# Kernel optimization log

Measured on AMD Instinct MI355X. Metric: run time of the kernel, lower is better.

Reference implementation:

```python
import jax, jax.numpy as jnp
import numpy as np

N, E = 20000, 320000
IN_DIM, CODE_DIM, HIDDEN, HEADS, NREL = 896, 768, 256, 4, 5
CH = HIDDEN // HEADS
CODE_WEIGHT = 3.0
NEG_SLOPE = 0.2


def _gat_layer(h, src, dst, W, att_src, att_dst, bias):
    # h: [N, HIDDEN]; src/dst already include self-loops. Eval mode -> no dropout.
    n = h.shape[0]
    x = (h @ W).reshape(n, HEADS, CH)                      # [N,H,C]
    a_src = (x * att_src).sum(-1)                          # [N,H]
    a_dst = (x * att_dst).sum(-1)                          # [N,H]
    alpha = jax.nn.leaky_relu(a_src[src] + a_dst[dst], NEG_SLOPE)  # [E',H]
    amax = jax.ops.segment_max(alpha, dst, num_segments=n)
    amax = jnp.where(jnp.isfinite(amax), amax, 0.0)
    ex = jnp.exp(alpha - amax[dst])
    denom = jax.ops.segment_sum(ex, dst, num_segments=n)
    coef = ex / denom[dst]                                 # segment softmax over in-neighbors
    msg = x[src] * coef[:, :, None]                        # [E',H,C]
    out = jax.ops.segment_sum(msg, dst, num_segments=n)    # [N,H,C]
    return out.reshape(n, HEADS * CH) + bias


def setup_inputs() -> dict:
    key = jax.random.key(0)
    ks = jax.random.split(key, 20)
    def glorot(k, shape):
        fan_in = shape[0]
        return jax.random.normal(k, shape, jnp.float32) / jnp.sqrt(jnp.asarray(fan_in, jnp.float32))
    inp = {
        "x": jax.random.normal(ks[0], (N, IN_DIM), jnp.float32),
        "edge_index": jax.random.randint(ks[1], (2, E), 0, N, jnp.int32),
        "edge_type": jax.random.randint(ks[2], (E,), 0, NREL, jnp.int32),
        "edge_weight": jax.random.uniform(ks[3], (E,), jnp.float32),
        "rel_emb": jax.random.normal(ks[4], (NREL, HIDDEN), jnp.float32),
        "Wp": glorot(ks[5], (IN_DIM, HIDDEN)),
        "bp": jnp.zeros((HIDDEN,), jnp.float32),
        "W1": glorot(ks[6], (HIDDEN, HIDDEN)),
        "att_src1": glorot(ks[7], (HEADS, CH)) * 0.1,
        "att_dst1": glorot(ks[8], (HEADS, CH)) * 0.1,
        "b1": jnp.zeros((HIDDEN,), jnp.float32),
        "W2": glorot(ks[9], (HIDDEN, HIDDEN)),
        "att_src2": glorot(ks[10], (HEADS, CH)) * 0.1,
        "att_dst2": glorot(ks[11], (HEADS, CH)) * 0.1,
        "b2": jnp.zeros((HIDDEN,), jnp.float32),
        "Wo": glorot(ks[12], (HIDDEN, 1)),
        "bo": jnp.zeros((1,), jnp.float32),
    }
    return inp


def reference(x, edge_index, edge_type, edge_weight, rel_emb, Wp, bp,
              W1, att_src1, att_dst1, b1, W2, att_src2, att_dst2, b2, Wo, bo):
    # feature reorder + code reweighting
    x_code = x[:, :CODE_DIM]
    x_num = x[:, CODE_DIM:]
    xc = jnp.concatenate([x_num, CODE_WEIGHT * x_code], axis=-1)
    h = jax.nn.relu(xc @ Wp + bp)                          # [N,HIDDEN]

    src, dst = edge_index[0], edge_index[1]
    # relational message + index_add scatter
    rel = rel_emb[edge_type] * edge_weight[:, None]        # [E,HIDDEN]
    msg = h[src] + rel
    h = h + jax.ops.segment_sum(msg, dst, num_segments=N)

    # GATConv adds self-loops by default
    loop = jnp.arange(N, dtype=src.dtype)
    src_sl = jnp.concatenate([src, loop])
    dst_sl = jnp.concatenate([dst, loop])

    h = _gat_layer(h, src_sl, dst_sl, W1, att_src1, att_dst1, b1)
    h = _gat_layer(h, src_sl, dst_sl, W2, att_src2, att_dst2, b2)
    score = (h @ Wo + bo)[:, 0]                            # [N]
    return score
```

## Files before the change

kernel.cpp:

```cpp
#include <hip/hip_runtime.h>
#include <hip/hip_bf16.h>

#define N_NODES 20000
#define E_EDGES 320000

typedef __attribute__((ext_vector_type(8))) short s8v;
typedef __attribute__((ext_vector_type(4))) float f4v;

__device__ __forceinline__ float lrelu(float v){ return v > 0.f ? v : 0.2f * v; }

__device__ __forceinline__ float bitf(unsigned short u){
  union { unsigned int i; float f; } v; v.i = ((unsigned int)u) << 16; return v.f;
}
__device__ __forceinline__ float4 bf4(const unsigned short* p){
  ushort4 u = *(const ushort4*)p;
  return make_float4(bitf(u.x), bitf(u.y), bitf(u.z), bitf(u.w));
}
__device__ __forceinline__ unsigned short bfhi(float v){
  union{float f; unsigned u;} a; a.f = v;
  unsigned r = a.u + 0x7FFFu + ((a.u >> 16) & 1u);
  return (unsigned short)(r >> 16);
}
__device__ __forceinline__ float bf2f(unsigned short h){
  union{unsigned u; float f;} a; a.u = ((unsigned)h) << 16; return a.f;
}
__device__ __forceinline__ void split2(float v0, float v1, unsigned& hu, unsigned& lu){
  __hip_bfloat162 h2 = __float22bfloat162_rn(make_float2(v0, v1));
  unsigned h; __builtin_memcpy(&h, &h2, 4);
  union{unsigned u; float f;} c0, c1;
  c0.u = h << 16;
  c1.u = h & 0xFFFF0000u;
  __hip_bfloat162 l2 = __float22bfloat162_rn(make_float2(v0 - c0.f, v1 - c1.f));
  unsigned l; __builtin_memcpy(&l, &l2, 4);
  hu = h; lu = l;
}
__device__ __forceinline__ void gl_lds16(const void* g, void* l){
  __builtin_amdgcn_global_load_lds(
      (const __attribute__((address_space(1))) unsigned int*)g,
      (__attribute__((address_space(3))) unsigned int*)l, 16, 0, 0);
}

__global__ __launch_bounds__(256) void k_count(const int* __restrict__ dst, int* __restrict__ deg, int E){
  int e = blockIdx.x * 256 + threadIdx.x;
  if (e < E) atomicAdd(&deg[dst[e]], 1);
}

__global__ __launch_bounds__(256) void k_scan(const int* __restrict__ deg, int* __restrict__ off,
                                              int* __restrict__ cur, int n){
  __shared__ int part[256];
  __shared__ int base[257];
  int tid = threadIdx.x;
  int chunk = (n + 255) / 256;
  int st = tid * chunk;
  int en = st + chunk; if (en > n) en = n;
  int s = 0;
  for (int i = st; i < en; ++i) s += deg[i];
  part[tid] = s;
  __syncthreads();
  if (tid == 0){
    int a = 0;
    for (int i = 0; i < 256; ++i){ base[i] = a; a += part[i]; }
    base[256] = a;
  }
  __syncthreads();
  int a = base[tid];
  for (int i = st; i < en; ++i){ off[i] = a; cur[i] = 0; a += deg[i]; }
  if (tid == 0) off[n] = base[256];
}

__global__ __launch_bounds__(256) void k_fill(const int* __restrict__ src, const int* __restrict__ dst,
                       const int* __restrict__ ety, const float* __restrict__ ew,
                       const int* __restrict__ off, int* __restrict__ cur,
                       int* __restrict__ csrc, int* __restrict__ cet, float* __restrict__ cw, int E){
  int e = blockIdx.x * 256 + threadIdx.x;
  if (e < E){
    int d = dst[e];
    int p = atomicAdd(&cur[d], 1);
    int i = off[d] + p;
    csrc[i] = src[e];
    cet[i]  = ety[e];
    cw[i]   = ew[e];
  }
}

__global__ __launch_bounds__(64) void k_prep(const float* __restrict__ W, unsigned short* __restrict__ Bp, int K){
  int kt = blockIdx.x;
  int n  = blockIdx.y * 64 + threadIdx.x;
  unsigned short hi[32], lo[32];
#pragma unroll
  for (int kk = 0; kk < 32; ++kk){
    float v = W[(size_t)(kt * 32 + kk) * 256 + n];
    unsigned short h = bfhi(v);
    hi[kk] = h;
    lo[kk] = bfhi(v - bf2f(h));
  }
  size_t plane = (size_t)(K >> 5) * 256 * 32;
  size_t b = ((size_t)kt * 256 + n) * 32;
#pragma unroll
  for (int kk = 0; kk < 32; ++kk){
    Bp[b + kk]         = hi[kk];
    Bp[plane + b + kk] = lo[kk];
  }
}

__global__ __launch_bounds__(128, 4) void k_mmp(
    const float* __restrict__ A, const unsigned short* __restrict__ Bp,
    const float* __restrict__ bias, unsigned short* __restrict__ Cout)
{
  constexpr int KT = 28;
  __shared__ unsigned short AhB[2][32 * 40];
  __shared__ unsigned short AlB[2][32 * 40];

  const int tid  = threadIdx.x;
  const int lane = tid & 63;
  const int wn   = tid >> 6;
  const int l15  = lane & 15;
  const int kg   = lane >> 4;
  const int m0   = blockIdx.x * 32;
  const int n0   = blockIdx.y * 128;
  const size_t planeB = (size_t)KT * 256 * 32;

  f4v acc[2][4];
#pragma unroll
  for (int f = 0; f < 2; ++f)
#pragma unroll
    for (int g = 0; g < 4; ++g)
#pragma unroll
      for (int r = 0; r < 4; ++r) acc[f][g][r] = 0.f;

  const int arow = tid >> 2;
  const int aj   = tid & 3;
  const int gr   = m0 + arow;

  auto loadA = [&](float* v, int kt){
    int c = kt * 32 + aj * 8;
    const float* sp; float sc;
    if (c < 128){ sp = A + (size_t)gr * 896 + (768 + c); sc = 1.f; }
    else        { sp = A + (size_t)gr * 896 + (c - 128); sc = 3.f; }
    float4 f0 = *(const float4*)sp;
    float4 f1 = *(const float4*)(sp + 4);
    v[0]=f0.x*sc; v[1]=f0.y*sc; v[2]=f0.z*sc; v[3]=f0.w*sc;
    v[4]=f1.x*sc; v[5]=f1.y*sc; v[6]=f1.z*sc; v[7]=f1.w*sc;
  };
  auto writeLDS = [&](const float* v, int buf){
    union { unsigned u[4]; s8v s; } hv, lv;
#pragma unroll
    for (int p = 0; p < 4; ++p)
      split2(v[2*p], v[2*p+1], hv.u[p], lv.u[p]);
    *(s8v*)&AhB[buf][arow * 40 + aj * 8] = hv.s;
    *(s8v*)&AlB[buf][arow * 40 + aj * 8] = lv.s;
  };

  float av[8];
  loadA(av, 0);
  writeLDS(av, 0);
  loadA(av, 1);

  int cur = 0;
#pragma unroll 1
  for (int kt = 0; kt < KT; ++kt){
    __syncthreads();
    if (kt + 1 < KT) writeLDS(av, cur ^ 1);
    if (kt + 2 < KT) loadA(av, kt + 2);
    s8v bh[4], bl[4];
#pragma unroll
    for (int g = 0; g < 4; ++g){
      const unsigned short* bp2 = Bp + ((size_t)kt * 256 + n0 + wn * 64 + g * 16 + l15) * 32 + kg * 8;
      bh[g] = *(const s8v*)bp2;
      bl[g] = *(const s8v*)(bp2 + planeB);
    }
    s8v ah[2], al[2];
#pragma unroll
    for (int f = 0; f < 2; ++f){
      int row = f * 16 + l15;
      ah[f] = *(const s8v*)&AhB[cur][row * 40 + kg * 8];
      al[f] = *(const s8v*)&AlB[cur][row * 40 + kg * 8];
    }
#pragma unroll
    for (int f = 0; f < 2; ++f)
#pragma unroll
      for (int g = 0; g < 4; ++g){
        acc[f][g] = __builtin_amdgcn_mfma_f32_16x16x32_bf16(ah[f], bh[g], acc[f][g], 0, 0, 0);
        acc[f][g] = __builtin_amdgcn_mfma_f32_16x16x32_bf16(ah[f], bl[g], acc[f][g], 0, 0, 0);
        acc[f][g] = __builtin_amdgcn_mfma_f32_16x16x32_bf16(al[f], bh[g], acc[f][g], 0, 0, 0);
      }
    cur ^= 1;
  }

#pragma unroll
  for (int f = 0; f < 2; ++f){
#pragma unroll
    for (int g = 0; g < 4; ++g){
      int col = n0 + wn * 64 + g * 16 + l15;
      float bb = bias[col];
#pragma unroll
      for (int r = 0; r < 4; ++r){
        int row = m0 + f * 16 + kg * 4 + r;
        float v = fmaxf(acc[f][g][r] + bb, 0.f);
        Cout[(size_t)row * 256 + col] = bfhi(v);
      }
    }
  }
}

__global__ __launch_bounds__(256, 2) void k_mmh(
    const unsigned short* __restrict__ Ahi, const unsigned short* __restrict__ Alo,
    const unsigned short* __restrict__ Bp, unsigned short* __restrict__ Cout,
    const float* __restrict__ attS, const float* __restrict__ attD,
    float* __restrict__ aS, float* __restrict__ aD)
{
  constexpr int KT = 8;
  __shared__ alignas(16) unsigned char Abuf[2][4096];

  const int tid  = threadIdx.x;
  const int lane = tid & 63;
  const int w    = tid >> 6;
  const int l15  = lane & 15;
  const int kg   = lane >> 4;
  const int m0   = blockIdx.x * 32;
  const size_t planeB = (size_t)KT * 256 * 32;

  f4v acc[2][4];
#pragma unroll
  for (int f = 0; f < 2; ++f)
#pragma unroll
    for (int g = 0; g < 4; ++g)
#pragma unroll
      for (int r = 0; r < 4; ++r) acc[f][g][r] = 0.f;

  auto stage = [&](int buf, int kt){
    int s   = tid;
    int p   = s >> 7;
    int sp  = s & 127;
    int row = sp >> 2;
    int kcp = sp & 3;
    int kc  = kcp ^ (row & 3);
    const unsigned short* basep = p ? Alo : Ahi;
    const unsigned short* gp = basep + (size_t)(m0 + row) * 256 + kt * 32 + kc * 8;
    gl_lds16(gp, &Abuf[buf][w * 1024]);
  };
  auto readFrags = [&](s8v* ah, s8v* al, int buf){
#pragma unroll
    for (int f = 0; f < 2; ++f){
      int row = f * 16 + l15;
      int kc  = kg ^ (row & 3);
      ah[f] = *(const s8v*)&Abuf[buf][row * 64 + kc * 16];
      al[f] = *(const s8v*)&Abuf[buf][2048 + row * 64 + kc * 16];
    }
  };
  auto loadB = [&](s8v* bh, s8v* bl, int kt){
#pragma unroll
    for (int g = 0; g < 4; ++g){
      const unsigned short* bp2 = Bp + ((size_t)kt * 256 + w * 64 + g * 16 + l15) * 32 + kg * 8;
      bh[g] = *(const s8v*)bp2;
      bl[g] = *(const s8v*)(bp2 + planeB);
    }
  };
  auto doMFMA = [&](const s8v* ah, const s8v* al, const s8v* bh, const s8v* bl){
#pragma unroll
    for (int f = 0; f < 2; ++f)
#pragma unroll
      for (int g = 0; g < 4; ++g){
        acc[f][g] = __builtin_amdgcn_mfma_f32_16x16x32_bf16(ah[f], bh[g], acc[f][g], 0, 0, 0);
        acc[f][g] = __builtin_amdgcn_mfma_f32_16x16x32_bf16(ah[f], bl[g], acc[f][g], 0, 0, 0);
        acc[f][g] = __builtin_amdgcn_mfma_f32_16x16x32_bf16(al[f], bh[g], acc[f][g], 0, 0, 0);
      }
  };

  s8v bh[4], bl[4];
  stage(0, 0);
  loadB(bh, bl, 0);
  __syncthreads();

  int cur = 0;
#pragma unroll 1
  for (int kt = 0; kt < KT; ++kt){
    if (kt + 1 < KT) stage(cur ^ 1, kt + 1);
    s8v ah[2], al[2];
    readFrags(ah, al, cur);
    s8v nbh[4], nbl[4];
    if (kt + 1 < KT) loadB(nbh, nbl, kt + 1);
    doMFMA(ah, al, bh, bl);
    if (kt + 1 < KT){
#pragma unroll
      for (int g = 0; g < 4; ++g){ bh[g] = nbh[g]; bl[g] = nbl[g]; }
    }
    __syncthreads();
    cur ^= 1;
  }

#pragma unroll
  for (int f = 0; f < 2; ++f){
#pragma unroll
    for (int g = 0; g < 4; ++g){
      int col = w * 64 + g * 16 + l15;
#pragma unroll
      for (int r = 0; r < 4; ++r){
        int row = m0 + f * 16 + kg * 4 + r;
        Cout[(size_t)row * 256 + col] = bfhi(acc[f][g][r]);
      }
    }
  }

  {
    const int head = w;
    float sv[4], dv[4];
#pragma unroll
    for (int g = 0; g < 4; ++g){
      int col = w * 64 + g * 16 + l15;
      sv[g] = attS[col];
      dv[g] = attD[col];
    }
#pragma unroll
    for (int f = 0; f < 2; ++f){
#pragma unroll
      for (int r = 0; r < 4; ++r){
        float ps = acc[f][0][r]*sv[0] + acc[f][1][r]*sv[1] + acc[f][2][r]*sv[2] + acc[f][3][r]*sv[3];
        float pd = acc[f][0][r]*dv[0] + acc[f][1][r]*dv[1] + acc[f][2][r]*dv[2] + acc[f][3][r]*dv[3];
#pragma unroll
        for (int mm = 1; mm < 16; mm <<= 1){
          ps += __shfl_xor(ps, mm, 64);
          pd += __shfl_xor(pd, mm, 64);
        }
        int row = m0 + f * 16 + kg * 4 + r;
        if (l15 == 0){
          aS[(size_t)row * 4 + head] = ps;
          aD[(size_t)row * 4 + head] = pd;
        }
      }
    }
  }
}

__global__ __launch_bounds__(256) void k_agg(
    const unsigned short* __restrict__ h0, const int* __restrict__ off,
    const int* __restrict__ csrc, const int* __restrict__ cet, const float* __restrict__ cw,
    const float* __restrict__ rel,
    unsigned short* __restrict__ h1hi, unsigned short* __restrict__ h1lo, int N)
{
  __shared__ int srcs[4][128];
  const int wv = threadIdx.x >> 6;
  const int n  = blockIdx.x * 4 + wv;
  if (n >= N) return;
  const int lane = threadIdx.x & 63;
  const int c0 = lane * 4;
  const int s0 = off[n], s1 = off[n + 1];
  const int deg = s1 - s0;
  const int nc = deg < 128 ? deg : 128;

  float w0=0.f, w1=0.f, w2=0.f, w3=0.f, w4=0.f;
  for (int base = 0; base < deg; base += 64){
    int ci = base + lane;
    if (ci < deg){
      int e = s0 + ci;
      int s = csrc[e];
      int t = cet[e];
      float wg = cw[e];
      if (ci < 128) srcs[wv][ci] = s;
      w0 += (t == 0) ? wg : 0.f;
      w1 += (t == 1) ? wg : 0.f;
      w2 += (t == 2) ? wg : 0.f;
      w3 += (t == 3) ? wg : 0.f;
      w4 += (t == 4) ? wg : 0.f;
    }
  }
#pragma unroll
  for (int mm = 1; mm < 64; mm <<= 1){
    w0 += __shfl_xor(w0, mm, 64);
    w1 += __shfl_xor(w1, mm, 64);
    w2 += __shfl_xor(w2, mm, 64);
    w3 += __shfl_xor(w3, mm, 64);
    w4 += __shfl_xor(w4, mm, 64);
  }
  asm volatile("s_waitcnt lgkmcnt(0)" ::: "memory");

  float4 acc = bf4(&h0[(size_t)n * 256 + c0]);
  { float4 R = *(const float4*)&rel[0 * 256 + c0];
    acc.x = fmaf(w0, R.x, acc.x); acc.y = fmaf(w0, R.y, acc.y);
    acc.z = fmaf(w0, R.z, acc.z); acc.w = fmaf(w0, R.w, acc.w); }
  { float4 R = *(const float4*)&rel[1 * 256 + c0];
    acc.x = fmaf(w1, R.x, acc.x); acc.y = fmaf(w1, R.y, acc.y);
    acc.z = fmaf(w1, R.z, acc.z); acc.w = fmaf(w1, R.w, acc.w); }
  { float4 R = *(const float4*)&rel[2 * 256 + c0];
    acc.x = fmaf(w2, R.x, acc.x); acc.y = fmaf(w2, R.y, acc.y);
    acc.z = fmaf(w2, R.z, acc.z); acc.w = fmaf(w2, R.w, acc.w); }
  { float4 R = *(const float4*)&rel[3 * 256 + c0];
    acc.x = fmaf(w3, R.x, acc.x); acc.y = fmaf(w3, R.y, acc.y);
    acc.z = fmaf(w3, R.z, acc.z); acc.w = fmaf(w3, R.w, acc.w); }
  { float4 R = *(const float4*)&rel[4 * 256 + c0];
    acc.x = fmaf(w4, R.x, acc.x); acc.y = fmaf(w4, R.y, acc.y);
    acc.z = fmaf(w4, R.z, acc.z); acc.w = fmaf(w4, R.w, acc.w); }

  int e = 0;
  for (; e + 7 < nc; e += 8){
    int sA = srcs[wv][e  ], sB = srcs[wv][e+1], sC = srcs[wv][e+2], sD = srcs[wv][e+3];
    int sE = srcs[wv][e+4], sF = srcs[wv][e+5], sG = srcs[wv][e+6], sH = srcs[wv][e+7];
    float4 xA = bf4(&h0[(size_t)sA * 256 + c0]);
    float4 xB = bf4(&h0[(size_t)sB * 256 + c0]);
    float4 xC = bf4(&h0[(size_t)sC * 256 + c0]);
    float4 xD = bf4(&h0[(size_t)sD * 256 + c0]);
    float4 xE = bf4(&h0[(size_t)sE * 256 + c0]);
    float4 xF = bf4(&h0[(size_t)sF * 256 + c0]);
    float4 xG = bf4(&h0[(size_t)sG * 256 + c0]);
    float4 xH = bf4(&h0[(size_t)sH * 256 + c0]);
    acc.x += ((xA.x + xB.x) + (xC.x + xD.x)) + ((xE.x + xF.x) + (xG.x + xH.x));
    acc.y += ((xA.y + xB.y) + (xC.y + xD.y)) + ((xE.y + xF.y) + (xG.y + xH.y));
    acc.z += ((xA.z + xB.z) + (xC.z + xD.z)) + ((xE.z + xF.z) + (xG.z + xH.z));
    acc.w += ((xA.w + xB.w) + (xC.w + xD.w)) + ((xE.w + xF.w) + (xG.w + xH.w));
  }
  for (; e < nc; ++e){
    int s = srcs[wv][e];
    float4 xv = bf4(&h0[(size_t)s * 256 + c0]);
    acc.x += xv.x; acc.y += xv.y; acc.z += xv.z; acc.w += xv.w;
  }
  for (int ci = 128; ci < deg; ++ci){
    int s = csrc[s0 + ci];
    float4 xv = bf4(&h0[(size_t)s * 256 + c0]);
    acc.x += xv.x; acc.y += xv.y; acc.z += xv.z; acc.w += xv.w;
  }

  ushort4 hi, lo;
  { unsigned short h;
    h = bfhi(acc.x); hi.x = h; lo.x = bfhi(acc.x - bf2f(h));
    h = bfhi(acc.y); hi.y = h; lo.y = bfhi(acc.y - bf2f(h));
    h = bfhi(acc.z); hi.z = h; lo.z = bfhi(acc.z - bf2f(h));
    h = bfhi(acc.w); hi.w = h; lo.w = bfhi(acc.w - bf2f(h));
  }
  *(ushort4*)&h1hi[(size_t)n * 256 + c0] = hi;
  *(ushort4*)&h1lo[(size_t)n * 256 + c0] = lo;
}

template<bool SCORE>
__global__ __launch_bounds__(256) void k_gat(
    const unsigned short* __restrict__ xh, const float* __restrict__ aS, const float* __restrict__ aD,
    const int* __restrict__ off, const int* __restrict__ csrc,
    const float* __restrict__ bias,
    unsigned short* __restrict__ h1hi, unsigned short* __restrict__ h1lo,
    const float* __restrict__ Wo, const float* __restrict__ bo, float* __restrict__ out, int N)
{
  __shared__ float4 exs[4][128];
  __shared__ int   srcs[4][128];
  const int wv   = threadIdx.x >> 6;
  const int n    = blockIdx.x * 4 + wv;
  if (n >= N) return;
  const int lane = threadIdx.x & 63;
  const int head = lane >> 4;
  const int c0   = lane * 4;
  const int s0 = off[n], s1 = off[n + 1];
  const int deg = s1 - s0;
  const int nc = deg < 128 ? deg : 128;

  float4 ad4 = *(const float4*)&aD[(size_t)n * 4];
  float4 asf = *(const float4*)&aS[(size_t)n * 4];
  float4 aself;
  aself.x = lrelu(asf.x + ad4.x); aself.y = lrelu(asf.y + ad4.y);
  aself.z = lrelu(asf.z + ad4.z); aself.w = lrelu(asf.w + ad4.w);
  float4 q = aself;

  for (int base = 0; base < deg; base += 64){
    int ci = base + lane;
    if (ci < deg){
      int s = csrc[s0 + ci];
      float4 av = *(const float4*)&aS[(size_t)s * 4];
      float4 al4;
      al4.x = lrelu(av.x + ad4.x); al4.y = lrelu(av.y + ad4.y);
      al4.z = lrelu(av.z + ad4.z); al4.w = lrelu(av.w + ad4.w);
      q.x = fmaxf(q.x, al4.x); q.y = fmaxf(q.y, al4.y);
      q.z = fmaxf(q.z, al4.z); q.w = fmaxf(q.w, al4.w);
      if (ci < 128){ srcs[wv][ci] = s; exs[wv][ci] = al4; }
    }
  }
#pragma unroll
  for (int mm = 1; mm < 64; mm <<= 1){
    q.x = fmaxf(q.x, __shfl_xor(q.x, mm, 64));
    q.y = fmaxf(q.y, __shfl_xor(q.y, mm, 64));
    q.z = fmaxf(q.z, __shfl_xor(q.z, mm, 64));
    q.w = fmaxf(q.w, __shfl_xor(q.w, mm, 64));
  }
  asm volatile("s_waitcnt lgkmcnt(0)" ::: "memory");

  float4 den4 = make_float4(0.f, 0.f, 0.f, 0.f);
  for (int ci = lane; ci < nc; ci += 64){
    float4 a = exs[wv][ci];
    float4 e4;
    e4.x = __expf(a.x - q.x); e4.y = __expf(a.y - q.y);
    e4.z = __expf(a.z - q.z); e4.w = __expf(a.w - q.w);
    exs[wv][ci] = e4;
    den4.x += e4.x; den4.y += e4.y; den4.z += e4.z; den4.w += e4.w;
  }
#pragma unroll
  for (int mm = 1; mm < 64; mm <<= 1){
    den4.x += __shfl_xor(den4.x, mm, 64);
    den4.y += __shfl_xor(den4.y, mm, 64);
    den4.z += __shfl_xor(den4.z, mm, 64);
    den4.w += __shfl_xor(den4.w, mm, 64);
  }
  asm volatile("s_waitcnt lgkmcnt(0)" ::: "memory");

  const float mh  = head == 0 ? q.x : (head == 1 ? q.y : (head == 2 ? q.z : q.w));
  const float adh = head == 0 ? ad4.x : (head == 1 ? ad4.y : (head == 2 ? ad4.z : ad4.w));
  const float aselfh = head == 0 ? aself.x : (head == 1 ? aself.y : (head == 2 ? aself.z : aself.w));
  float den = (head == 0 ? den4.x : (head == 1 ? den4.y : (head == 2 ? den4.z : den4.w)));
  float exself = __expf(aselfh - mh);
  den += exself;

  float4 xv = bf4(&xh[(size_t)n * 256 + c0]);
  float4 acc;
  acc.x = exself * xv.x; acc.y = exself * xv.y; acc.z = exself * xv.z; acc.w = exself * xv.w;

  const float* exw = (const float*)&exs[wv][0];
  int e = 0;
  for (; e + 7 < nc; e += 8){
    int sA = srcs[wv][e  ], sB = srcs[wv][e+1], sC = srcs[wv][e+2], sD = srcs[wv][e+3];
    int sE = srcs[wv][e+4], sF = srcs[wv][e+5], sG = srcs[wv][e+6], sH = srcs[wv][e+7];
    float eA = exw[(e  ) * 4 + head], eB = exw[(e+1) * 4 + head];
    float eC = exw[(e+2) * 4 + head], eD = exw[(e+3) * 4 + head];
    float eE = exw[(e+4) * 4 + head], eF = exw[(e+5) * 4 + head];
    float eG = exw[(e+6) * 4 + head], eH = exw[(e+7) * 4 + head];
    float4 xA = bf4(&xh[(size_t)sA * 256 + c0]);
    float4 xB = bf4(&xh[(size_t)sB * 256 + c0]);
    float4 xC = bf4(&xh[(size_t)sC * 256 + c0]);
    float4 xD = bf4(&xh[(size_t)sD * 256 + c0]);
    float4 xE = bf4(&xh[(size_t)sE * 256 + c0]);
    float4 xF = bf4(&xh[(size_t)sF * 256 + c0]);
    float4 xG = bf4(&xh[(size_t)sG * 256 + c0]);
    float4 xH = bf4(&xh[(size_t)sH * 256 + c0]);
    float t0, t1, t2, t3;
    t0 = eA*xA.x + eB*xB.x; t1 = eC*xC.x + eD*xD.x; t2 = eE*xE.x + eF*xF.x; t3 = eG*xG.x + eH*xH.x;
    acc.x += (t0 + t1) + (t2 + t3);
    t0 = eA*xA.y + eB*xB.y; t1 = eC*xC.y + eD*xD.y; t2 = eE*xE.y + eF*xF.y; t3 = eG*xG.y + eH*xH.y;
    acc.y += (t0 + t1) + (t2 + t3);
    t0 = eA*xA.z + eB*xB.z; t1 = eC*xC.z + eD*xD.z; t2 = eE*xE.z + eF*xF.z; t3 = eG*xG.z + eH*xH.z;
    acc.z += (t0 + t1) + (t2 + t3);
    t0 = eA*xA.w + eB*xB.w; t1 = eC*xC.w + eD*xD.w; t2 = eE*xE.w + eF*xF.w; t3 = eG*xG.w + eH*xH.w;
    acc.w += (t0 + t1) + (t2 + t3);
  }
  for (; e < nc; ++e){
    int s = srcs[wv][e];
    float ef = exw[e * 4 + head];
    float4 x2 = bf4(&xh[(size_t)s * 256 + c0]);
    acc.x = fmaf(ef, x2.x, acc.x);
    acc.y = fmaf(ef, x2.y, acc.y);
    acc.z = fmaf(ef, x2.z, acc.z);
    acc.w = fmaf(ef, x2.w, acc.w);
  }
  for (int ci = 128; ci < deg; ++ci){
    int s = csrc[s0 + ci];
    float a  = aS[(size_t)s * 4 + head];
    float ef = __expf(lrelu(a + adh) - mh);
    den += ef;
    float4 x2 = bf4(&xh[(size_t)s * 256 + c0]);
    acc.x = fmaf(ef, x2.x, acc.x);
    acc.y = fmaf(ef, x2.y, acc.y);
    acc.z = fmaf(ef, x2.z, acc.z);
    acc.w = fmaf(ef, x2.w, acc.w);
  }

  float inv = 1.f / den;
  float4 bb = *(const float4*)&bias[c0];
  float4 o;
  o.x = acc.x * inv + bb.x;
  o.y = acc.y * inv + bb.y;
  o.z = acc.z * inv + bb.z;
  o.w = acc.w * inv + bb.w;
  if constexpr (SCORE){
    float4 wvv = *(const float4*)&Wo[c0];
    float p = o.x * wvv.x + o.y * wvv.y + o.z * wvv.z + o.w * wvv.w;
#pragma unroll
    for (int mm = 1; mm < 64; mm <<= 1) p += __shfl_xor(p, mm, 64);
    if (lane == 0) out[n] = p + bo[0];
  } else {
    ushort4 hi, lo;
    unsigned short h;
    h = bfhi(o.x); hi.x = h; lo.x = bfhi(o.x - bf2f(h));
    h = bfhi(o.y); hi.y = h; lo.y = bfhi(o.y - bf2f(h));
    h = bfhi(o.z); hi.z = h; lo.z = bfhi(o.z - bf2f(h));
    h = bfhi(o.w); hi.w = h; lo.w = bfhi(o.w - bf2f(h));
    *(ushort4*)&h1hi[(size_t)n * 256 + c0] = hi;
    *(ushort4*)&h1lo[(size_t)n * 256 + c0] = lo;
  }
}

extern "C" void kernel_launch(void* const* d_in, const int* in_sizes, int n_in,
                              void* d_out, int out_size, void* d_ws, size_t ws_size,
                              hipStream_t stream)
{
  const float* x   = (const float*)d_in[0];
  const int*   ei  = (const int*)  d_in[1];
  const int*   ety = (const int*)  d_in[2];
  const float* ew  = (const float*)d_in[3];
  const float* rel = (const float*)d_in[4];
  const float* Wp  = (const float*)d_in[5];
  const float* bp  = (const float*)d_in[6];
  const float* W1  = (const float*)d_in[7];
  const float* as1 = (const float*)d_in[8];
  const float* ad1 = (const float*)d_in[9];
  const float* b1  = (const float*)d_in[10];
  const float* W2  = (const float*)d_in[11];
  const float* as2 = (const float*)d_in[12];
  const float* ad2 = (const float*)d_in[13];
  const float* b2  = (const float*)d_in[14];
  const float* Wo  = (const float*)d_in[15];
  const float* bo  = (const float*)d_in[16];
  float* out = (float*)d_out;

  const int N = N_NODES, E = E_EDGES;
  char* w = (char*)d_ws;
  size_t o = 0;
  auto alloc = [&](size_t bytes) -> char* {
    char* p = w + o;
    o = (o + bytes + 255) & ~(size_t)255;
    return p;
  };
  unsigned short* h0b  = (unsigned short*)alloc((size_t)N * 256 * 2);
  unsigned short* xhb  = (unsigned short*)alloc((size_t)N * 256 * 2);
  unsigned short* h1hi = (unsigned short*)alloc((size_t)N * 256 * 2);
  unsigned short* h1lo = (unsigned short*)alloc((size_t)N * 256 * 2);
  float* aS  = (float*)alloc((size_t)N * 4 * 4);
  float* aD  = (float*)alloc((size_t)N * 4 * 4);
  int* deg   = (int*)alloc((size_t)N * 4);
  int* offs  = (int*)alloc((size_t)(N + 1) * 4);
  int* cur   = (int*)alloc((size_t)N * 4);
  int* csrc  = (int*)alloc((size_t)E * 4);
  int* cet   = (int*)alloc((size_t)E * 4);
  float* cw  = (float*)alloc((size_t)E * 4);
  unsigned short* BpP = (unsigned short*)alloc((size_t)2 * 896 * 256 * 2);
  unsigned short* Bp1 = (unsigned short*)alloc((size_t)2 * 256 * 256 * 2);
  unsigned short* Bp2 = (unsigned short*)alloc((size_t)2 * 256 * 256 * 2);

  const int* srcp = ei;
  const int* dstp = ei + E;

  hipMemsetAsync(deg, 0, (size_t)N * 4, stream);
  k_count<<<(E + 255) / 256, 256, 0, stream>>>(dstp, deg, E);
  k_scan<<<1, 256, 0, stream>>>(deg, offs, cur, N);
  k_fill<<<(E + 255) / 256, 256, 0, stream>>>(srcp, dstp, ety, ew, offs, cur, csrc, cet, cw, E);

  k_prep<<<dim3(896 / 32, 4), 64, 0, stream>>>(Wp, BpP, 896);
  k_prep<<<dim3(256 / 32, 4), 64, 0, stream>>>(W1, Bp1, 256);
  k_prep<<<dim3(256 / 32, 4), 64, 0, stream>>>(W2, Bp2, 256);

  const int gmm = N_NODES / 32;
  int nblk = (N + 3) / 4;

  k_mmp<<<dim3(gmm, 2), 128, 0, stream>>>(x, BpP, bp, h0b);
  k_agg<<<nblk, 256, 0, stream>>>(h0b, offs, csrc, cet, cw, rel, h1hi, h1lo, N);
  k_mmh<<<gmm, 256, 0, stream>>>(h1hi, h1lo, Bp1, xhb, as1, ad1, aS, aD);
  k_gat<false><<<nblk, 256, 0, stream>>>(xhb, aS, aD, offs, csrc, b1, h1hi, h1lo, nullptr, nullptr, nullptr, N);
  k_mmh<<<gmm, 256, 0, stream>>>(h1hi, h1lo, Bp2, xhb, as2, ad2, aS, aD);
  k_gat<true><<<nblk, 256, 0, stream>>>(xhb, aS, aD, offs, csrc, b2, nullptr, nullptr, Wo, bo, out, N);
}
```

Baseline: 276.6 us.

## Split input projection GEMM along K and reduce partials in separate kernel

The input projection GEMM now splits its K dimension across two z-blocks. Each block writes fp32 partial sums to a workspace buffer, and a new reduction kernel adds the partials, applies bias and ReLU, and stores bf16. The goal is to double the block count for more parallelism across CUs. In exchange it adds about 40MB of fp32 partial traffic and one extra kernel launch.

```diff
diff --git a/kernel.cpp b/kernel.cpp
--- a/kernel.cpp
+++ b/kernel.cpp
@@ -103,11 +103,11 @@
   }
 }
 
-__global__ __launch_bounds__(128, 4) void k_mmp(
+__global__ __launch_bounds__(128, 4) void k_mmps(
     const float* __restrict__ A, const unsigned short* __restrict__ Bp,
-    const float* __restrict__ bias, unsigned short* __restrict__ Cout)
+    float* __restrict__ P)
 {
-  constexpr int KT = 28;
+  constexpr int KTH = 14;
   __shared__ unsigned short AhB[2][32 * 40];
   __shared__ unsigned short AlB[2][32 * 40];
 
@@ -118,7 +118,8 @@
   const int kg   = lane >> 4;
   const int m0   = blockIdx.x * 32;
   const int n0   = blockIdx.y * 128;
-  const size_t planeB = (size_t)KT * 256 * 32;
+  const int kt0  = blockIdx.z * KTH;
+  const size_t planeB = (size_t)28 * 256 * 32;
 
   f4v acc[2][4];
 #pragma unroll
@@ -152,16 +153,17 @@
   };
 
   float av[8];
-  loadA(av, 0);
+  loadA(av, kt0);
   writeLDS(av, 0);
-  loadA(av, 1);
+  loadA(av, kt0 + 1);
 
   int cur = 0;
 #pragma unroll 1
-  for (int kt = 0; kt < KT; ++kt){
+  for (int t = 0; t < KTH; ++t){
+    const int kt = kt0 + t;
     __syncthreads();
-    if (kt + 1 < KT) writeLDS(av, cur ^ 1);
-    if (kt + 2 < KT) loadA(av, kt + 2);
+    if (t + 1 < KTH) writeLDS(av, cur ^ 1);
+    if (t + 2 < KTH) loadA(av, kt + 2);
     s8v bh[4], bl[4];
 #pragma unroll
     for (int g = 0; g < 4; ++g){
@@ -187,20 +189,37 @@
     cur ^= 1;
   }
 
+  float* Pz = P + (size_t)blockIdx.z * N_NODES * 256;
 #pragma unroll
   for (int f = 0; f < 2; ++f){
 #pragma unroll
     for (int g = 0; g < 4; ++g){
       int col = n0 + wn * 64 + g * 16 + l15;
-      float bb = bias[col];
 #pragma unroll
       for (int r = 0; r < 4; ++r){
         int row = m0 + f * 16 + kg * 4 + r;
-        float v = fmaxf(acc[f][g][r] + bb, 0.f);
-        Cout[(size_t)row * 256 + col] = bfhi(v);
+        Pz[(size_t)row * 256 + col] = acc[f][g][r];
       }
     }
   }
+}
+
+__global__ __launch_bounds__(256) void k_red(
+    const float* __restrict__ P, const float* __restrict__ bias,
+    unsigned short* __restrict__ h0)
+{
+  size_t t = (size_t)blockIdx.x * 256 + threadIdx.x;
+  size_t i = t * 4;
+  int col = (int)(i & 255);
+  float4 p0 = *(const float4*)&P[i];
+  float4 p1 = *(const float4*)&P[(size_t)N_NODES * 256 + i];
+  float4 bb = *(const float4*)&bias[col];
+  ushort4 o;
+  o.x = bfhi(fmaxf(p0.x + p1.x + bb.x, 0.f));
+  o.y = bfhi(fmaxf(p0.y + p1.y + bb.y, 0.f));
+  o.z = bfhi(fmaxf(p0.z + p1.z + bb.z, 0.f));
+  o.w = bfhi(fmaxf(p0.w + p1.w + bb.w, 0.f));
+  *(ushort4*)&h0[i] = o;
 }
 
 __global__ __launch_bounds__(256, 2) void k_mmh(
@@ -616,6 +635,7 @@
   unsigned short* xhb  = (unsigned short*)alloc((size_t)N * 256 * 2);
   unsigned short* h1hi = (unsigned short*)alloc((size_t)N * 256 * 2);
   unsigned short* h1lo = (unsigned short*)alloc((size_t)N * 256 * 2);
+  float* Ppart = (float*)alloc((size_t)2 * N * 256 * 4);
   float* aS  = (float*)alloc((size_t)N * 4 * 4);
   float* aD  = (float*)alloc((size_t)N * 4 * 4);
   int* deg   = (int*)alloc((size_t)N * 4);
@@ -643,7 +663,8 @@
   const int gmm = N_NODES / 32;
   int nblk = (N + 3) / 4;
 
-  k_mmp<<<dim3(gmm, 2), 128, 0, stream>>>(x, BpP, bp, h0b);
+  k_mmps<<<dim3(gmm, 2, 2), 128, 0, stream>>>(x, BpP, Ppart);
+  k_red<<<(N * 256) / (256 * 4), 256, 0, stream>>>(Ppart, bp, h0b);
   k_agg<<<nblk, 256, 0, stream>>>(h0b, offs, csrc, cet, cw, rel, h1hi, h1lo, N);
   k_mmh<<<gmm, 256, 0, stream>>>(h1hi, h1lo, Bp1, xhb, as1, ad1, aS, aD);
   k_gat<false><<<nblk, 256, 0, stream>>>(xhb, aS, aD, offs, csrc, b1, h1hi, h1lo, nullptr, nullptr, nullptr, N);
```

After: 285.8 us. 1.03x slower.

## Enlarge input projection GEMM tile, deepen prefetch, fold code scale into weights

Applied to the files above, without the earlier changes.

The input projection GEMM now uses 64-row tiles with four waves in a 2x2 arrangement instead of 32-row tiles with two waves. It also prefetches A three k-steps ahead and B one step ahead in registers. The x3 code-feature scaling moves out of the per-element A load and into the weight split kernel. The aim is to reuse B tiles across more rows, hide global load latency, and cut ALU work in the inner loop, at the cost of higher register pressure and lower occupancy. Rows past N are clamped on load and masked on store.

```diff
diff --git a/kernel.cpp b/kernel.cpp
--- a/kernel.cpp
+++ b/kernel.cpp
@@ -83,13 +83,16 @@
   }
 }
 
+template<bool SC3>
 __global__ __launch_bounds__(64) void k_prep(const float* __restrict__ W, unsigned short* __restrict__ Bp, int K){
   int kt = blockIdx.x;
   int n  = blockIdx.y * 64 + threadIdx.x;
   unsigned short hi[32], lo[32];
 #pragma unroll
   for (int kk = 0; kk < 32; ++kk){
-    float v = W[(size_t)(kt * 32 + kk) * 256 + n];
+    int krow = kt * 32 + kk;
+    float v = W[(size_t)krow * 256 + n];
+    if constexpr (SC3){ if (krow >= 128) v *= 3.0f; }
     unsigned short h = bfhi(v);
     hi[kk] = h;
     lo[kk] = bfhi(v - bf2f(h));
@@ -103,20 +106,22 @@
   }
 }
 
-__global__ __launch_bounds__(128, 4) void k_mmp(
+__global__ __launch_bounds__(256, 3) void k_mmq(
     const float* __restrict__ A, const unsigned short* __restrict__ Bp,
     const float* __restrict__ bias, unsigned short* __restrict__ Cout)
 {
   constexpr int KT = 28;
-  __shared__ unsigned short AhB[2][32 * 40];
-  __shared__ unsigned short AlB[2][32 * 40];
+  __shared__ unsigned short Ah[2][64 * 40];
+  __shared__ unsigned short Al[2][64 * 40];
 
   const int tid  = threadIdx.x;
   const int lane = tid & 63;
-  const int wn   = tid >> 6;
+  const int w    = tid >> 6;
+  const int wm   = w >> 1;
+  const int wn   = w & 1;
   const int l15  = lane & 15;
   const int kg   = lane >> 4;
-  const int m0   = blockIdx.x * 32;
+  const int m0   = blockIdx.x * 64;
   const int n0   = blockIdx.y * 128;
   const size_t planeB = (size_t)KT * 256 * 32;
 
@@ -130,51 +135,60 @@
 
   const int arow = tid >> 2;
   const int aj   = tid & 3;
-  const int gr   = m0 + arow;
+  int grr = m0 + arow; if (grr > N_NODES - 1) grr = N_NODES - 1;
+  const int gr   = grr;
 
   auto loadA = [&](float* v, int kt){
     int c = kt * 32 + aj * 8;
-    const float* sp; float sc;
-    if (c < 128){ sp = A + (size_t)gr * 896 + (768 + c); sc = 1.f; }
-    else        { sp = A + (size_t)gr * 896 + (c - 128); sc = 3.f; }
+    const float* sp = (c < 128) ? (A + (size_t)gr * 896 + (768 + c))
+                                : (A + (size_t)gr * 896 + (c - 128));
     float4 f0 = *(const float4*)sp;
     float4 f1 = *(const float4*)(sp + 4);
-    v[0]=f0.x*sc; v[1]=f0.y*sc; v[2]=f0.z*sc; v[3]=f0.w*sc;
-    v[4]=f1.x*sc; v[5]=f1.y*sc; v[6]=f1.z*sc; v[7]=f1.w*sc;
-  };
-  auto writeLDS = [&](const float* v, int buf){
+    v[0]=f0.x; v[1]=f0.y; v[2]=f0.z; v[3]=f0.w;
+    v[4]=f1.x; v[5]=f1.y; v[6]=f1.z; v[7]=f1.w;
+  };
+  auto writeL = [&](const float* v, int buf){
     union { unsigned u[4]; s8v s; } hv, lv;
 #pragma unroll
     for (int p = 0; p < 4; ++p)
       split2(v[2*p], v[2*p+1], hv.u[p], lv.u[p]);
-    *(s8v*)&AhB[buf][arow * 40 + aj * 8] = hv.s;
-    *(s8v*)&AlB[buf][arow * 40 + aj * 8] = lv.s;
-  };
-
-  float av[8];
-  loadA(av, 0);
-  writeLDS(av, 0);
-  loadA(av, 1);
-
-  int cur = 0;
-#pragma unroll 1
-  for (int kt = 0; kt < KT; ++kt){
-    __syncthreads();
-    if (kt + 1 < KT) writeLDS(av, cur ^ 1);
-    if (kt + 2 < KT) loadA(av, kt + 2);
-    s8v bh[4], bl[4];
+    *(s8v*)&Ah[buf][arow * 40 + aj * 8] = hv.s;
+    *(s8v*)&Al[buf][arow * 40 + aj * 8] = lv.s;
+  };
+  auto loadB = [&](s8v* bh, s8v* bl, int kt){
 #pragma unroll
     for (int g = 0; g < 4; ++g){
       const unsigned short* bp2 = Bp + ((size_t)kt * 256 + n0 + wn * 64 + g * 16 + l15) * 32 + kg * 8;
       bh[g] = *(const s8v*)bp2;
       bl[g] = *(const s8v*)(bp2 + planeB);
     }
+  };
+
+  float a1[8], a2[8], an[8];
+  {
+    float a0[8];
+    loadA(a0, 0);
+    writeL(a0, 0);
+  }
+  loadA(a1, 1);
+  loadA(a2, 2);
+  s8v bh[4], bl[4], nbh[4], nbl[4];
+  loadB(bh, bl, 0);
+
+  int cur = 0;
+#pragma unroll 1
+  for (int kt = 0; kt < KT; ++kt){
+    asm volatile("s_waitcnt lgkmcnt(0)" ::: "memory");
+    __builtin_amdgcn_s_barrier();
+    if (kt + 1 < KT) writeL(a1, cur ^ 1);
+    if (kt + 3 < KT) loadA(an, kt + 3);
+    if (kt + 1 < KT) loadB(nbh, nbl, kt + 1);
     s8v ah[2], al[2];
 #pragma unroll
     for (int f = 0; f < 2; ++f){
-      int row = f * 16 + l15;
-      ah[f] = *(const s8v*)&AhB[cur][row * 40 + kg * 8];
-      al[f] = *(const s8v*)&AlB[cur][row * 40 + kg * 8];
+      int row = wm * 32 + f * 16 + l15;
+      ah[f] = *(const s8v*)&Ah[cur][row * 40 + kg * 8];
+      al[f] = *(const s8v*)&Al[cur][row * 40 + kg * 8];
     }
 #pragma unroll
     for (int f = 0; f < 2; ++f)
@@ -184,6 +198,10 @@
         acc[f][g] = __builtin_amdgcn_mfma_f32_16x16x32_bf16(ah[f], bl[g], acc[f][g], 0, 0, 0);
         acc[f][g] = __builtin_amdgcn_mfma_f32_16x16x32_bf16(al[f], bh[g], acc[f][g], 0, 0, 0);
       }
+#pragma unroll
+    for (int j = 0; j < 8; ++j){ a1[j] = a2[j]; a2[j] = an[j]; }
+#pragma unroll
+    for (int g = 0; g < 4; ++g){ bh[g] = nbh[g]; bl[g] = nbl[g]; }
     cur ^= 1;
   }
 
@@ -195,9 +213,11 @@
       float bb = bias[col];
 #pragma unroll
       for (int r = 0; r < 4; ++r){
-        int row = m0 + f * 16 + kg * 4 + r;
-        float v = fmaxf(acc[f][g][r] + bb, 0.f);
-        Cout[(size_t)row * 256 + col] = bfhi(v);
+        int row = m0 + wm * 32 + f * 16 + kg * 4 + r;
+        if (row < N_NODES){
+          float v = fmaxf(acc[f][g][r] + bb, 0.f);
+          Cout[(size_t)row * 256 + col] = bfhi(v);
+        }
       }
     }
   }
@@ -636,14 +656,14 @@
   k_scan<<<1, 256, 0, stream>>>(deg, offs, cur, N);
   k_fill<<<(E + 255) / 256, 256, 0, stream>>>(srcp, dstp, ety, ew, offs, cur, csrc, cet, cw, E);
 
-  k_prep<<<dim3(896 / 32, 4), 64, 0, stream>>>(Wp, BpP, 896);
-  k_prep<<<dim3(256 / 32, 4), 64, 0, stream>>>(W1, Bp1, 256);
-  k_prep<<<dim3(256 / 32, 4), 64, 0, stream>>>(W2, Bp2, 256);
+  k_prep<true ><<<dim3(896 / 32, 4), 64, 0, stream>>>(Wp, BpP, 896);
+  k_prep<false><<<dim3(256 / 32, 4), 64, 0, stream>>>(W1, Bp1, 256);
+  k_prep<false><<<dim3(256 / 32, 4), 64, 0, stream>>>(W2, Bp2, 256);
 
   const int gmm = N_NODES / 32;
   int nblk = (N + 3) / 4;
 
-  k_mmp<<<dim3(gmm, 2), 128, 0, stream>>>(x, BpP, bp, h0b);
+  k_mmq<<<dim3((N_NODES + 63) / 64, 2), 256, 0, stream>>>(x, BpP, bp, h0b);
   k_agg<<<nblk, 256, 0, stream>>>(h0b, offs, csrc, cet, cw, rel, h1hi, h1lo, N);
   k_mmh<<<gmm, 256, 0, stream>>>(h1hi, h1lo, Bp1, xhb, as1, ad1, aS, aD);
   k_gat<false><<<nblk, 256, 0, stream>>>(xhb, aS, aD, offs, csrc, b1, h1hi, h1lo, nullptr, nullptr, nullptr, N);
```

Result: slower. 283.0 us (+2.3%).
